# Kernel tuning notes

Measured on AMD Instinct MI355X. Metric: run time of the kernel, lower is better.

## Reference

```python
import jax, jax.numpy as jnp
import numpy as np

B = 16      # number of point clouds in the batch
N = 2048    # points per cloud
P = B * N   # total points (flat PyG-style batching)
K = 16      # neighbors per point (col 0 = self loop)
OUT = 512   # out_channels


def _linear(key, fi, fo):
    # torch nn.Linear default init: U(-1/sqrt(fi), 1/sqrt(fi))
    s = 1.0 / np.sqrt(fi)
    kw, kb = jax.random.split(key)
    W = jax.random.uniform(kw, (fi, fo), jnp.float32, -s, s)
    b = jax.random.uniform(kb, (fo,), jnp.float32, -s, s)
    return W, b


def setup_inputs() -> dict:
    key = jax.random.key(0)
    ks = jax.random.split(key, 6)
    pos = jax.random.normal(ks[0], (P, 3), jnp.float32)
    # flat batch vector: points are grouped contiguously per cloud
    batch = (jnp.arange(P, dtype=jnp.int32) // N).astype(jnp.int32)
    # within-cloud random neighbor indices (stand-in for knn/radius graph)
    base = (jnp.arange(P) // N) * N  # offset of each point's cloud
    nbr = base[:, None] + jax.random.randint(ks[1], (P, K), 0, N)
    nbr = nbr.at[:, 0].set(jnp.arange(P))  # self loop (PyG add_self_loops)
    W1, b1 = _linear(ks[2], 3, 64)          # sa1 MLP layer 1
    W2, b2 = _linear(ks[3], 64, 128)        # sa1 MLP layer 2
    W3, b3 = _linear(ks[4], 128 + 3, 256)   # sa2 MLP layer 1
    W4, b4 = _linear(ks[5], 256, OUT)       # sa2 MLP layer 2
    return dict(pos=pos, nbr=nbr.astype(jnp.int64), batch=batch,
                W1=W1, b1=b1, W2=W2, b2=b2, W3=W3, b3=b3, W4=W4, b4=b4)


def reference(pos, nbr, batch, W1, b1, W2, b2, W3, b3, W4, b4):
    # ----- sa1: x is None -> message = MLP(pos_j - pos_i), max-aggregated -----
    diff = pos[nbr] - pos[:, None, :]                      # [P, K, 3]
    h1 = jnp.maximum(diff @ W1 + b1, 0.0) @ W2 + b2        # [P, K, 128]
    x1 = jnp.max(h1, axis=1)                               # [P, 128]
    # ----- sa2: message = MLP([x1_j, pos_j - pos_i]), max-aggregated -----
    feats = jnp.concatenate([x1[nbr], diff], axis=-1)      # [P, K, 131]
    h2 = jnp.maximum(feats @ W3 + b3, 0.0) @ W4 + b4       # [P, K, 512]
    x2 = jnp.max(h2, axis=1)                               # [P, 512]
    # ----- global_max_pool over batch -----
    return jax.ops.segment_max(x2, batch, num_segments=B)  # [B, 512]
```

## Files before the change

### kernel.cpp

```cpp
#include <hip/hip_runtime.h>
#include <hip/hip_bf16.h>

#define PTOT   32768
#define KNB    16
#define NCLOUD 16
#define OUTC   512
#define A1S    168
#define A2S    264

typedef __attribute__((ext_vector_type(8)))  short v8bf;
typedef __attribute__((ext_vector_type(16))) float v16f;

__device__ __forceinline__ unsigned short f2b(float v) {
    __hip_bfloat16 h = __float2bfloat16(v);
    return *reinterpret_cast<unsigned short*>(&h);
}
__device__ __forceinline__ unsigned pk2(float a, float b) {
    return (unsigned)f2b(a) | ((unsigned)f2b(b) << 16);
}
__device__ __forceinline__ unsigned fenc(float f) {
    unsigned u = __float_as_uint(f);
    return (u & 0x80000000u) ? ~u : (u | 0x80000000u);
}
__device__ __forceinline__ float fdec(unsigned u) {
    unsigned b = (u & 0x80000000u) ? (u & 0x7FFFFFFFu) : ~u;
    return __uint_as_float(b);
}
__device__ __forceinline__ v16f zero16() {
    v16f z;
    #pragma unroll
    for (int i = 0; i < 16; ++i) z[i] = 0.0f;
    return z;
}

__global__ void prep_kernel(const float* __restrict__ W1, const float* __restrict__ W2,
                            const float* __restrict__ W3, const float* __restrict__ W4,
                            unsigned short* __restrict__ W1s, unsigned short* __restrict__ W2s,
                            unsigned short* __restrict__ W3s, unsigned short* __restrict__ W4s)
{
    int i = blockIdx.x * 256 + threadIdx.x;
    if (i < 40960) {
        int j = i & 7, n = (i >> 3) & 255, c2 = i >> 11;
        int k = c2 * 8 + j;
        W3s[i] = f2b(k < 131 ? W3[k * 256 + n] : 0.0f);
    }
    int i2 = i - 40960;
    if (i2 >= 0 && i2 < 131072) {
        int j = i2 & 7, n = (i2 >> 3) & 511, c2 = i2 >> 12;
        int k = c2 * 8 + j;
        W4s[i2] = f2b(W4[k * 512 + n]);
    }
    int i3 = i - 172032;
    if (i3 >= 0 && i3 < 1024) {
        int k = i3 & 15, n = i3 >> 4;
        W1s[i3] = f2b(k < 3 ? W1[k * 64 + n] : 0.0f);
    }
    int i4 = i - 173056;
    if (i4 >= 0 && i4 < 8192) {
        int k = i4 & 63, n = i4 >> 6;
        W2s[i4] = f2b(W2[k * 128 + n]);
    }
}

__global__ __launch_bounds__(256) void sa1_kernel(
    const float* __restrict__ pos, const int* __restrict__ nbr,
    const unsigned short* __restrict__ W1s, const float* __restrict__ b1,
    const unsigned short* __restrict__ W2s, const float* __restrict__ b2,
    unsigned short* __restrict__ x1b)
{
    __shared__ unsigned short A1d[64 * 16];
    __shared__ unsigned short A2[64 * 72];
    const int tid  = threadIdx.x;
    const int lane = tid & 63;
    const int wave = tid >> 6;
    const int l31  = lane & 31;
    const int h    = lane >> 5;
    const int p0   = blockIdx.x * 4;

    if (tid < 64) {
        int r = tid;
        int j = nbr[p0 * KNB + r];
        int p = p0 + (r >> 4);
        v8bf z;
        #pragma unroll
        for (int i = 0; i < 8; ++i) z[i] = 0;
        v8bf dv = z;
        dv[0] = (short)f2b(pos[j * 3 + 0] - pos[p * 3 + 0]);
        dv[1] = (short)f2b(pos[j * 3 + 1] - pos[p * 3 + 1]);
        dv[2] = (short)f2b(pos[j * 3 + 2] - pos[p * 3 + 2]);
        *(v8bf*)(A1d + r * 16)     = dv;
        *(v8bf*)(A1d + r * 16 + 8) = z;
    }
    const int c1 = (wave >> 1) * 32 + l31;
    v8bf b1f = *(const v8bf*)(W1s + c1 * 16 + h * 8);
    const float b1v = b1[c1];
    __syncthreads();

    {
        v8bf a = *(const v8bf*)(A1d + ((wave & 1) * 32 + l31) * 16 + h * 8);
        v16f acc = __builtin_amdgcn_mfma_f32_32x32x16_bf16(a, b1f, zero16(), 0, 0, 0);
        #pragma unroll
        for (int r = 0; r < 16; ++r) {
            int row = (wave & 1) * 32 + (r & 3) + 8 * (r >> 2) + 4 * h;
            A2[row * 72 + c1] = f2b(fmaxf(acc[r] + b1v, 0.0f));
        }
    }
    v8bf B2[4];
    #pragma unroll
    for (int kc = 0; kc < 4; ++kc)
        B2[kc] = *(const v8bf*)(W2s + (wave * 32 + l31) * 64 + kc * 16 + h * 8);
    const float b2v = b2[wave * 32 + l31];
    __syncthreads();

    #pragma unroll
    for (int rt = 0; rt < 2; ++rt) {
        v16f acc = zero16();
        #pragma unroll
        for (int kc = 0; kc < 4; ++kc) {
            v8bf a = *(const v8bf*)(A2 + (rt * 32 + l31) * 72 + kc * 16 + h * 8);
            acc = __builtin_amdgcn_mfma_f32_32x32x16_bf16(a, B2[kc], acc, 0, 0, 0);
        }
        float ma = acc[0], mb = acc[8];
        #pragma unroll
        for (int r = 1; r < 8; ++r) { ma = fmaxf(ma, acc[r]); mb = fmaxf(mb, acc[8 + r]); }
        ma = fmaxf(ma, __shfl_xor(ma, 32));
        mb = fmaxf(mb, __shfl_xor(mb, 32));
        int p = p0 + rt * 2 + h;
        float m = h ? mb : ma;
        x1b[p * 128 + wave * 32 + l31] = f2b(m + b2v);
    }
}

__global__ __launch_bounds__(256) void sa2_kernel(
    const float* __restrict__ pos, const int* __restrict__ nbr,
    const int* __restrict__ batch,
    const unsigned short* __restrict__ W3s, const float* __restrict__ b3,
    const unsigned short* __restrict__ W4s, const float* __restrict__ b4,
    const unsigned short* __restrict__ x1b, unsigned* __restrict__ encbuf)
{
    __shared__ unsigned short S[64 * A2S];
    const int tid  = threadIdx.x;
    const int lane = tid & 63;
    const int wave = tid >> 6;
    const int l31  = lane & 31;
    const int h    = lane >> 5;
    const int p0   = blockIdx.x * 4;

    const float b3v0 = b3[(wave * 2 + 0) * 32 + l31];
    const float b3v1 = b3[(wave * 2 + 1) * 32 + l31];

    {
        int r = tid >> 2, q4 = tid & 3;
        int j = nbr[p0 * KNB + r];
        const uint4* src = (const uint4*)(x1b + j * 128 + q4 * 32);
        uint4* dst = (uint4*)(S + r * A1S + q4 * 32);
        dst[0] = src[0]; dst[1] = src[1]; dst[2] = src[2]; dst[3] = src[3];
    }
    if (tid < 64) {
        int r = tid;
        int j = nbr[p0 * KNB + r];
        int p = p0 + (r >> 4);
        v8bf z;
        #pragma unroll
        for (int i = 0; i < 8; ++i) z[i] = 0;
        v8bf dv = z;
        dv[0] = (short)f2b(pos[j * 3 + 0] - pos[p * 3 + 0]);
        dv[1] = (short)f2b(pos[j * 3 + 1] - pos[p * 3 + 1]);
        dv[2] = (short)f2b(pos[j * 3 + 2] - pos[p * 3 + 2]);
        *(v8bf*)(S + r * A1S + 128) = dv;
        *(v8bf*)(S + r * A1S + 136) = z;
        *(v8bf*)(S + r * A1S + 144) = z;
        *(v8bf*)(S + r * A1S + 152) = z;
    }
    __syncthreads();

    v16f g00 = zero16(), g01 = zero16(), g10 = zero16(), g11 = zero16();
    const int n1a = (wave * 2 + 0) * 32 + l31;
    const int n1b = (wave * 2 + 1) * 32 + l31;
    #pragma unroll
    for (int kc = 0; kc < 9; ++kc) {
        v8bf a0 = *(const v8bf*)(S + (l31)      * A1S + kc * 16 + h * 8);
        v8bf a1 = *(const v8bf*)(S + (32 + l31) * A1S + kc * 16 + h * 8);
        int c2 = kc * 2 + h;
        v8bf B0 = *(const v8bf*)(W3s + ((c2 * 256 + n1a) << 3));
        v8bf B1 = *(const v8bf*)(W3s + ((c2 * 256 + n1b) << 3));
        g00 = __builtin_amdgcn_mfma_f32_32x32x16_bf16(a0, B0, g00, 0, 0, 0);
        g10 = __builtin_amdgcn_mfma_f32_32x32x16_bf16(a1, B0, g10, 0, 0, 0);
        g01 = __builtin_amdgcn_mfma_f32_32x32x16_bf16(a0, B1, g01, 0, 0, 0);
        g11 = __builtin_amdgcn_mfma_f32_32x32x16_bf16(a1, B1, g11, 0, 0, 0);
    }
    unsigned st[2][16];
    #pragma unroll
    for (int i = 0; i < 8; ++i) {
        st[0][i]     = pk2(fmaxf(g00[2 * i] + b3v0, 0.0f), fmaxf(g00[2 * i + 1] + b3v0, 0.0f));
        st[0][8 + i] = pk2(fmaxf(g10[2 * i] + b3v0, 0.0f), fmaxf(g10[2 * i + 1] + b3v0, 0.0f));
        st[1][i]     = pk2(fmaxf(g01[2 * i] + b3v1, 0.0f), fmaxf(g01[2 * i + 1] + b3v1, 0.0f));
        st[1][8 + i] = pk2(fmaxf(g11[2 * i] + b3v1, 0.0f), fmaxf(g11[2 * i + 1] + b3v1, 0.0f));
    }
    __syncthreads();

    #pragma unroll
    for (int ci = 0; ci < 2; ++ci) {
        int c = (wave * 2 + ci) * 32 + l31;
        #pragma unroll
        for (int i = 0; i < 8; ++i) {
            int row = ((2 * i) & 3) + 8 * ((2 * i) >> 2) + 4 * h;
            S[row * A2S + c]            = (unsigned short)(st[ci][i] & 0xFFFF);
            S[(row + 1) * A2S + c]      = (unsigned short)(st[ci][i] >> 16);
            S[(32 + row) * A2S + c]     = (unsigned short)(st[ci][8 + i] & 0xFFFF);
            S[(32 + row + 1) * A2S + c] = (unsigned short)(st[ci][8 + i] >> 16);
        }
    }
    __syncthreads();

    const int cloud = batch[p0];
    #pragma unroll
    for (int pass = 0; pass < 2; ++pass) {
        const int ct0 = wave * 4 + pass * 2;
        const int n0 = ct0 * 32 + l31;
        const int n1 = (ct0 + 1) * 32 + l31;
        v16f a00 = zero16(), a01 = zero16(), a10 = zero16(), a11 = zero16();
        #pragma unroll
        for (int kc = 0; kc < 16; ++kc) {
            v8bf a0 = *(const v8bf*)(S + (l31)      * A2S + kc * 16 + h * 8);
            v8bf a1 = *(const v8bf*)(S + (32 + l31) * A2S + kc * 16 + h * 8);
            int c2 = kc * 2 + h;
            v8bf Ba = *(const v8bf*)(W4s + ((c2 * 512 + n0) << 3));
            v8bf Bb = *(const v8bf*)(W4s + ((c2 * 512 + n1) << 3));
            a00 = __builtin_amdgcn_mfma_f32_32x32x16_bf16(a0, Ba, a00, 0, 0, 0);
            a10 = __builtin_amdgcn_mfma_f32_32x32x16_bf16(a1, Ba, a10, 0, 0, 0);
            a01 = __builtin_amdgcn_mfma_f32_32x32x16_bf16(a0, Bb, a01, 0, 0, 0);
            a11 = __builtin_amdgcn_mfma_f32_32x32x16_bf16(a1, Bb, a11, 0, 0, 0);
        }
        float m0 = a00[0], m1 = a01[0];
        #pragma unroll
        for (int r = 1; r < 16; ++r) { m0 = fmaxf(m0, a00[r]); m1 = fmaxf(m1, a01[r]); }
        #pragma unroll
        for (int r = 0; r < 16; ++r) { m0 = fmaxf(m0, a10[r]); m1 = fmaxf(m1, a11[r]); }
        m0 = fmaxf(m0, __shfl_xor(m0, 32));
        m1 = fmaxf(m1, __shfl_xor(m1, 32));
        m0 += b4[ct0 * 32 + l31];
        m1 += b4[(ct0 + 1) * 32 + l31];
        if (lane < 32) {
            atomicMax(&encbuf[cloud * OUTC + ct0 * 32 + l31], fenc(m0));
            atomicMax(&encbuf[cloud * OUTC + (ct0 + 1) * 32 + l31], fenc(m1));
        }
    }
}

__global__ void finalize_kernel(const unsigned* __restrict__ encv,
                                float* __restrict__ out)
{
    int i = blockIdx.x * 256 + threadIdx.x;
    if (i < NCLOUD * OUTC) out[i] = fdec(encv[i]);
}

extern "C" void kernel_launch(void* const* d_in, const int* in_sizes, int n_in,
                              void* d_out, int out_size, void* d_ws, size_t ws_size,
                              hipStream_t stream)
{
    const float* pos   = (const float*)d_in[0];
    const int*   nbr   = (const int*)  d_in[1];
    const int*   batch = (const int*)  d_in[2];
    const float* W1    = (const float*)d_in[3];
    const float* b1    = (const float*)d_in[4];
    const float* W2    = (const float*)d_in[5];
    const float* b2    = (const float*)d_in[6];
    const float* W3    = (const float*)d_in[7];
    const float* b3    = (const float*)d_in[8];
    const float* W4    = (const float*)d_in[9];
    const float* b4    = (const float*)d_in[10];

    unsigned short* x1b = (unsigned short*)d_ws;
    unsigned short* W3s = (unsigned short*)((char*)d_ws + 8388608);
    unsigned short* W4s = (unsigned short*)((char*)d_ws + 8470528);
    unsigned*    encbuf = (unsigned*)((char*)d_ws + 8732672);
    unsigned short* W1s = (unsigned short*)((char*)d_ws + 8765440);
    unsigned short* W2s = (unsigned short*)((char*)d_ws + 8767488);

    hipMemsetAsync(encbuf, 0, NCLOUD * OUTC * sizeof(unsigned), stream);
    prep_kernel<<<708, 256, 0, stream>>>(W1, W2, W3, W4, W1s, W2s, W3s, W4s);
    sa1_kernel<<<PTOT / 4, 256, 0, stream>>>(pos, nbr, W1s, b1, W2s, b2, x1b);
    sa2_kernel<<<PTOT / 4, 256, 0, stream>>>(pos, nbr, batch, W3s, b3, W4s, b4, x1b, encbuf);
    finalize_kernel<<<(NCLOUD * OUTC + 255) / 256, 256, 0, stream>>>(encbuf, (float*)d_out);
}
```

Before: 288.1 us.

## Process eight points per sa2 block and keep W4 fragments in registers

```diff
diff --git a/kernel.cpp b/kernel.cpp
--- a/kernel.cpp
+++ b/kernel.cpp
@@ -138,25 +138,26 @@
     const unsigned short* __restrict__ W4s, const float* __restrict__ b4,
     const unsigned short* __restrict__ x1b, unsigned* __restrict__ encbuf)
 {
-    __shared__ unsigned short S[64 * A2S];
+    __shared__ unsigned short S[128 * A2S];
     const int tid  = threadIdx.x;
     const int lane = tid & 63;
     const int wave = tid >> 6;
     const int l31  = lane & 31;
     const int h    = lane >> 5;
-    const int p0   = blockIdx.x * 4;
+    const int p0   = blockIdx.x * 8;
 
     const float b3v0 = b3[(wave * 2 + 0) * 32 + l31];
     const float b3v1 = b3[(wave * 2 + 1) * 32 + l31];
 
     {
-        int r = tid >> 2, q4 = tid & 3;
+        int r = tid >> 1, q = tid & 1;
         int j = nbr[p0 * KNB + r];
-        const uint4* src = (const uint4*)(x1b + j * 128 + q4 * 32);
-        uint4* dst = (uint4*)(S + r * A1S + q4 * 32);
-        dst[0] = src[0]; dst[1] = src[1]; dst[2] = src[2]; dst[3] = src[3];
-    }
-    if (tid < 64) {
+        const uint4* src = (const uint4*)(x1b + j * 128 + q * 64);
+        uint4* dst = (uint4*)(S + r * A1S + q * 64);
+        #pragma unroll
+        for (int i = 0; i < 8; ++i) dst[i] = src[i];
+    }
+    if (tid < 128) {
         int r = tid;
         int j = nbr[p0 * KNB + r];
         int p = p0 + (r >> 4);
@@ -169,81 +170,98 @@
         dv[2] = (short)f2b(pos[j * 3 + 2] - pos[p * 3 + 2]);
         *(v8bf*)(S + r * A1S + 128) = dv;
         *(v8bf*)(S + r * A1S + 136) = z;
-        *(v8bf*)(S + r * A1S + 144) = z;
-        *(v8bf*)(S + r * A1S + 152) = z;
-    }
-    __syncthreads();
-
-    v16f g00 = zero16(), g01 = zero16(), g10 = zero16(), g11 = zero16();
+    }
+    __syncthreads();
+
     const int n1a = (wave * 2 + 0) * 32 + l31;
     const int n1b = (wave * 2 + 1) * 32 + l31;
-    #pragma unroll
-    for (int kc = 0; kc < 9; ++kc) {
-        v8bf a0 = *(const v8bf*)(S + (l31)      * A1S + kc * 16 + h * 8);
-        v8bf a1 = *(const v8bf*)(S + (32 + l31) * A1S + kc * 16 + h * 8);
-        int c2 = kc * 2 + h;
-        v8bf B0 = *(const v8bf*)(W3s + ((c2 * 256 + n1a) << 3));
-        v8bf B1 = *(const v8bf*)(W3s + ((c2 * 256 + n1b) << 3));
-        g00 = __builtin_amdgcn_mfma_f32_32x32x16_bf16(a0, B0, g00, 0, 0, 0);
-        g10 = __builtin_amdgcn_mfma_f32_32x32x16_bf16(a1, B0, g10, 0, 0, 0);
-        g01 = __builtin_amdgcn_mfma_f32_32x32x16_bf16(a0, B1, g01, 0, 0, 0);
-        g11 = __builtin_amdgcn_mfma_f32_32x32x16_bf16(a1, B1, g11, 0, 0, 0);
-    }
-    unsigned st[2][16];
-    #pragma unroll
-    for (int i = 0; i < 8; ++i) {
-        st[0][i]     = pk2(fmaxf(g00[2 * i] + b3v0, 0.0f), fmaxf(g00[2 * i + 1] + b3v0, 0.0f));
-        st[0][8 + i] = pk2(fmaxf(g10[2 * i] + b3v0, 0.0f), fmaxf(g10[2 * i + 1] + b3v0, 0.0f));
-        st[1][i]     = pk2(fmaxf(g01[2 * i] + b3v1, 0.0f), fmaxf(g01[2 * i + 1] + b3v1, 0.0f));
-        st[1][8 + i] = pk2(fmaxf(g11[2 * i] + b3v1, 0.0f), fmaxf(g11[2 * i + 1] + b3v1, 0.0f));
-    }
-    __syncthreads();
-
-    #pragma unroll
-    for (int ci = 0; ci < 2; ++ci) {
-        int c = (wave * 2 + ci) * 32 + l31;
+    unsigned stA[2][16], stB[2][16];
+    #pragma unroll
+    for (int rtp = 0; rtp < 2; ++rtp) {
+        v16f g00 = zero16(), g01 = zero16(), g10 = zero16(), g11 = zero16();
+        #pragma unroll
+        for (int kc = 0; kc < 9; ++kc) {
+            v8bf a0 = *(const v8bf*)(S + (rtp * 64 + l31)      * A1S + kc * 16 + h * 8);
+            v8bf a1 = *(const v8bf*)(S + (rtp * 64 + 32 + l31) * A1S + kc * 16 + h * 8);
+            int c2 = kc * 2 + h;
+            v8bf B0 = *(const v8bf*)(W3s + ((c2 * 256 + n1a) << 3));
+            v8bf B1 = *(const v8bf*)(W3s + ((c2 * 256 + n1b) << 3));
+            g00 = __builtin_amdgcn_mfma_f32_32x32x16_bf16(a0, B0, g00, 0, 0, 0);
+            g10 = __builtin_amdgcn_mfma_f32_32x32x16_bf16(a1, B0, g10, 0, 0, 0);
+            g01 = __builtin_amdgcn_mfma_f32_32x32x16_bf16(a0, B1, g01, 0, 0, 0);
+            g11 = __builtin_amdgcn_mfma_f32_32x32x16_bf16(a1, B1, g11, 0, 0, 0);
+        }
         #pragma unroll
         for (int i = 0; i < 8; ++i) {
-            int row = ((2 * i) & 3) + 8 * ((2 * i) >> 2) + 4 * h;
-            S[row * A2S + c]            = (unsigned short)(st[ci][i] & 0xFFFF);
-            S[(row + 1) * A2S + c]      = (unsigned short)(st[ci][i] >> 16);
-            S[(32 + row) * A2S + c]     = (unsigned short)(st[ci][8 + i] & 0xFFFF);
-            S[(32 + row + 1) * A2S + c] = (unsigned short)(st[ci][8 + i] >> 16);
+            stA[rtp][i]     = pk2(fmaxf(g00[2*i] + b3v0, 0.0f), fmaxf(g00[2*i+1] + b3v0, 0.0f));
+            stA[rtp][8 + i] = pk2(fmaxf(g10[2*i] + b3v0, 0.0f), fmaxf(g10[2*i+1] + b3v0, 0.0f));
+            stB[rtp][i]     = pk2(fmaxf(g01[2*i] + b3v1, 0.0f), fmaxf(g01[2*i+1] + b3v1, 0.0f));
+            stB[rtp][8 + i] = pk2(fmaxf(g11[2*i] + b3v1, 0.0f), fmaxf(g11[2*i+1] + b3v1, 0.0f));
+        }
+    }
+    __syncthreads();
+
+    {
+        const int c0 = (wave * 2 + 0) * 32 + l31;
+        const int c1 = (wave * 2 + 1) * 32 + l31;
+        #pragma unroll
+        for (int rtp = 0; rtp < 2; ++rtp) {
+            const int rb = rtp * 64;
+            #pragma unroll
+            for (int i = 0; i < 8; ++i) {
+                int row = rb + ((2*i) & 3) + 8 * ((2*i) >> 2) + 4 * h;
+                S[row * A2S + c0]        = (unsigned short)(stA[rtp][i] & 0xFFFF);
+                S[(row + 1) * A2S + c0]  = (unsigned short)(stA[rtp][i] >> 16);
+                S[(row + 32) * A2S + c0] = (unsigned short)(stA[rtp][8 + i] & 0xFFFF);
+                S[(row + 33) * A2S + c0] = (unsigned short)(stA[rtp][8 + i] >> 16);
+                S[row * A2S + c1]        = (unsigned short)(stB[rtp][i] & 0xFFFF);
+                S[(row + 1) * A2S + c1]  = (unsigned short)(stB[rtp][i] >> 16);
+                S[(row + 32) * A2S + c1] = (unsigned short)(stB[rtp][8 + i] & 0xFFFF);
+                S[(row + 33) * A2S + c1] = (unsigned short)(stB[rtp][8 + i] >> 16);
+            }
         }
     }
     __syncthreads();
 
     const int cloud = batch[p0];
     #pragma unroll
-    for (int pass = 0; pass < 2; ++pass) {
-        const int ct0 = wave * 4 + pass * 2;
+    for (int cp = 0; cp < 2; ++cp) {
+        const int ct0 = wave * 4 + cp * 2;
         const int n0 = ct0 * 32 + l31;
         const int n1 = (ct0 + 1) * 32 + l31;
-        v16f a00 = zero16(), a01 = zero16(), a10 = zero16(), a11 = zero16();
+        v8bf B2a[16], B2b[16];
         #pragma unroll
         for (int kc = 0; kc < 16; ++kc) {
-            v8bf a0 = *(const v8bf*)(S + (l31)      * A2S + kc * 16 + h * 8);
-            v8bf a1 = *(const v8bf*)(S + (32 + l31) * A2S + kc * 16 + h * 8);
             int c2 = kc * 2 + h;
-            v8bf Ba = *(const v8bf*)(W4s + ((c2 * 512 + n0) << 3));
-            v8bf Bb = *(const v8bf*)(W4s + ((c2 * 512 + n1) << 3));
-            a00 = __builtin_amdgcn_mfma_f32_32x32x16_bf16(a0, Ba, a00, 0, 0, 0);
-            a10 = __builtin_amdgcn_mfma_f32_32x32x16_bf16(a1, Ba, a10, 0, 0, 0);
-            a01 = __builtin_amdgcn_mfma_f32_32x32x16_bf16(a0, Bb, a01, 0, 0, 0);
-            a11 = __builtin_amdgcn_mfma_f32_32x32x16_bf16(a1, Bb, a11, 0, 0, 0);
-        }
-        float m0 = a00[0], m1 = a01[0];
-        #pragma unroll
-        for (int r = 1; r < 16; ++r) { m0 = fmaxf(m0, a00[r]); m1 = fmaxf(m1, a01[r]); }
-        #pragma unroll
-        for (int r = 0; r < 16; ++r) { m0 = fmaxf(m0, a10[r]); m1 = fmaxf(m1, a11[r]); }
-        m0 = fmaxf(m0, __shfl_xor(m0, 32));
-        m1 = fmaxf(m1, __shfl_xor(m1, 32));
-        m0 += b4[ct0 * 32 + l31];
-        m1 += b4[(ct0 + 1) * 32 + l31];
+            B2a[kc] = *(const v8bf*)(W4s + ((c2 * 512 + n0) << 3));
+            B2b[kc] = *(const v8bf*)(W4s + ((c2 * 512 + n1) << 3));
+        }
+        float rm0 = -3.4e38f, rm1 = -3.4e38f;
+        #pragma unroll
+        for (int rtp = 0; rtp < 2; ++rtp) {
+            v16f a00 = zero16(), a01 = zero16(), a10 = zero16(), a11 = zero16();
+            #pragma unroll
+            for (int kc = 0; kc < 16; ++kc) {
+                v8bf a0 = *(const v8bf*)(S + (rtp * 64 + l31)      * A2S + kc * 16 + h * 8);
+                v8bf a1 = *(const v8bf*)(S + (rtp * 64 + 32 + l31) * A2S + kc * 16 + h * 8);
+                a00 = __builtin_amdgcn_mfma_f32_32x32x16_bf16(a0, B2a[kc], a00, 0, 0, 0);
+                a10 = __builtin_amdgcn_mfma_f32_32x32x16_bf16(a1, B2a[kc], a10, 0, 0, 0);
+                a01 = __builtin_amdgcn_mfma_f32_32x32x16_bf16(a0, B2b[kc], a01, 0, 0, 0);
+                a11 = __builtin_amdgcn_mfma_f32_32x32x16_bf16(a1, B2b[kc], a11, 0, 0, 0);
+            }
+            #pragma unroll
+            for (int r = 0; r < 16; ++r) {
+                rm0 = fmaxf(rm0, fmaxf(a00[r], a10[r]));
+                rm1 = fmaxf(rm1, fmaxf(a01[r], a11[r]));
+            }
+        }
+        rm0 = fmaxf(rm0, __shfl_xor(rm0, 32));
+        rm1 = fmaxf(rm1, __shfl_xor(rm1, 32));
+        rm0 += b4[ct0 * 32 + l31];
+        rm1 += b4[(ct0 + 1) * 32 + l31];
         if (lane < 32) {
-            atomicMax(&encbuf[cloud * OUTC + ct0 * 32 + l31], fenc(m0));
-            atomicMax(&encbuf[cloud * OUTC + (ct0 + 1) * 32 + l31], fenc(m1));
+            atomicMax(&encbuf[cloud * OUTC + ct0 * 32 + l31], fenc(rm0));
+            atomicMax(&encbuf[cloud * OUTC + (ct0 + 1) * 32 + l31], fenc(rm1));
         }
     }
 }
@@ -281,6 +299,6 @@
     hipMemsetAsync(encbuf, 0, NCLOUD * OUTC * sizeof(unsigned), stream);
     prep_kernel<<<708, 256, 0, stream>>>(W1, W2, W3, W4, W1s, W2s, W3s, W4s);
     sa1_kernel<<<PTOT / 4, 256, 0, stream>>>(pos, nbr, W1s, b1, W2s, b2, x1b);
-    sa2_kernel<<<PTOT / 4, 256, 0, stream>>>(pos, nbr, batch, W3s, b3, W4s, b4, x1b, encbuf);
+    sa2_kernel<<<PTOT / 8, 256, 0, stream>>>(pos, nbr, batch, W3s, b3, W4s, b4, x1b, encbuf);
     finalize_kernel<<<(NCLOUD * OUTC + 255) / 256, 256, 0, stream>>>(encbuf, (float*)d_out);
 }
```

Measured after the change: 252.7 us. 12.3% less time.
